# Kernel tuning notes

Measured on AMD Instinct MI355X. Metric: run time of the kernel, lower is better.

Reference implementation:

```python
import jax, jax.numpy as jnp
import numpy as np

N = 20000      # n_nodes
E = 320000     # n_edges (avg degree 16)
DIM = 64       # feature dim
HEADS = 4      # attention heads; per-head channel = DIM (PyG TransformerConv with concat=False)


def setup_inputs() -> dict:
    key = jax.random.key(0)
    ks = jax.random.split(key, 12)
    s = 0.05
    return {
        "f_mole": jax.random.normal(ks[0], (N, DIM), jnp.float32),
        "edge_weight": jax.random.uniform(ks[1], (E,), jnp.float32),
        "gcn_w": jax.random.normal(ks[2], (DIM, DIM), jnp.float32) * s,
        "gcn_b": jnp.zeros((DIM,), jnp.float32),
        "wq": jax.random.normal(ks[3], (DIM, HEADS * DIM), jnp.float32) * s,
        "bq": jnp.zeros((HEADS * DIM,), jnp.float32),
        "wk": jax.random.normal(ks[4], (DIM, HEADS * DIM), jnp.float32) * s,
        "bk": jnp.zeros((HEADS * DIM,), jnp.float32),
        "wv": jax.random.normal(ks[5], (DIM, HEADS * DIM), jnp.float32) * s,
        "bv": jnp.zeros((HEADS * DIM,), jnp.float32),
        "wskip": jax.random.normal(ks[6], (DIM, DIM), jnp.float32) * s,
        "bskip": jnp.zeros((DIM,), jnp.float32),
        "wbeta": jax.random.normal(ks[7], (3 * DIM, 1), jnp.float32) * s,
        "conv_w": jax.random.normal(ks[8], (DIM, DIM), jnp.float32) * s,  # Conv1d weight[o,0,k,0]
        "conv_b": jnp.zeros((DIM,), jnp.float32),
        "edges": jax.random.randint(ks[9], (2, E), 0, N, jnp.int32),
    }


def _forward(f_mole, edge_weight, gcn_w, gcn_b, wq, bq, wk, bk, wv, bv,
             wskip, bskip, wbeta, conv_w, conv_b, edges):
    n = f_mole.shape[0]
    dim = f_mole.shape[1]
    heads = wq.shape[1] // dim
    src, dst = edges[0], edges[1]  # PyG flow: source -> target

    # ---- GCNConv(dim, dim) with edge weights (add_self_loops=True, normalize=True) ----
    loops = jnp.arange(n, dtype=src.dtype)
    src_sl = jnp.concatenate([src, loops])
    dst_sl = jnp.concatenate([dst, loops])
    ew = jnp.concatenate([edge_weight, jnp.ones((n,), f_mole.dtype)])
    deg = jax.ops.segment_sum(ew, dst_sl, num_segments=n)
    dinv = jnp.where(deg > 0, jax.lax.rsqrt(deg), 0.0)
    norm = dinv[src_sl] * ew * dinv[dst_sl]              # (E+N,)
    xw = f_mole @ gcn_w                                   # (N, dim)
    agg = jax.ops.segment_sum(norm[:, None] * xw[src_sl], dst_sl, num_segments=n)
    f_gcn = jax.nn.relu(agg + gcn_b)                      # (N, dim)

    # ---- TransformerConv(dim, dim, heads, concat=False, beta=True) ----
    q = (f_gcn @ wq + bq).reshape(n, heads, dim)
    k = (f_gcn @ wk + bk).reshape(n, heads, dim)
    v = (f_gcn @ wv + bv).reshape(n, heads, dim)
    logits = jnp.einsum('ehc,ehc->eh', q[dst], k[src]) / jnp.sqrt(jnp.float32(dim))  # (E, H)
    m = jax.ops.segment_max(logits, dst, num_segments=n)  # (N, H)
    ex = jnp.exp(logits - m[dst])
    z = jax.ops.segment_sum(ex, dst, num_segments=n)      # (N, H)
    alpha = ex / z[dst]                                   # per-target softmax over edges
    out = jax.ops.segment_sum(alpha[:, :, None] * v[src], dst, num_segments=n)  # (N, H, dim)
    out = out.mean(axis=1)                                # concat=False -> head mean
    x_r = f_gcn @ wskip + bskip                           # root/skip branch
    beta = jax.nn.sigmoid(jnp.concatenate([out, x_r, out - x_r], axis=-1) @ wbeta)  # (N, 1)
    f_tf = jax.nn.relu(beta * x_r + (1.0 - beta) * out)   # (N, dim)

    # ---- Conv1d(1, dim, kernel_size=(dim,1)) on f_tf.T viewed as (1,1,dim,N) ----
    # out[o, n] = sum_k conv_w[o, k] * f_tf.T[k, n] + conv_b[o]  -> shape (1, dim, 1, N)
    conv = jnp.einsum('ok,nk->on', conv_w, f_tf) + conv_b[:, None]  # (dim, N)
    # torch .view(1, n_mole, -1) on (1, dim, 1, N): row-major reshape
    f_intra = conv.reshape(1, n, dim)
    return f_intra


def reference(f_mole, edge_weight, gcn_w, gcn_b, wq, bq, wk, bk, wv, bv,
              wskip, bskip, wbeta, conv_w, conv_b, edges):
    return _forward(f_mole, edge_weight, gcn_w, gcn_b, wq, bq, wk, bk, wv, bv,
                    wskip, bskip, wbeta, conv_w, conv_b, edges)
```

## Files before the change

kernel.cpp:

```cpp
#include <hip/hip_runtime.h>
#include <hip/hip_bf16.h>

#define DIM 64
#define HEADS 4
#define HD 256
#define CAP 64

typedef __attribute__((ext_vector_type(8))) short bf16x8;
typedef __attribute__((ext_vector_type(8))) unsigned short u16x8;
typedef __attribute__((ext_vector_type(4))) float f32x4;

template<int CTRL>
__device__ __forceinline__ float dpp_rot(float x) {
    return __int_as_float(__builtin_amdgcn_update_dpp(
        0, __float_as_int(x), CTRL, 0xF, 0xF, true));
}
__device__ __forceinline__ float reduce16(float x) {
    x += dpp_rot<0x121>(x);
    x += dpp_rot<0x122>(x);
    x += dpp_rot<0x124>(x);
    x += dpp_rot<0x128>(x);
    return x;
}
__device__ __forceinline__ unsigned short f2bf(float f) {
    unsigned u = __float_as_uint(f);
    unsigned r = (u + 0x7FFFu + ((u >> 16) & 1u)) >> 16;
    return (unsigned short)r;
}
__device__ __forceinline__ float bf2f(unsigned short u) {
    return __uint_as_float((unsigned)u << 16);
}

__global__ void scatter_all(const int* __restrict__ edges, const float* __restrict__ ew,
                            int* counts, int2* __restrict__ csr, int nE) {
    int e = blockIdx.x * blockDim.x + threadIdx.x;
    if (e < nE) {
        int dst = edges[nE + e];
        int src = edges[e];
        float w = ew[e];
        int p = atomicAdd(&counts[dst], 1);
        int2 rec;
        rec.x = src;
        rec.y = __float_as_int(w);
        csr[(dst << 6) + p] = rec;
    }
}

__global__ __launch_bounds__(256) void deg_dinv_k(const int* __restrict__ counts,
                                                  const int2* __restrict__ csr,
                                                  float* __restrict__ dinv, int n) {
    int i = blockIdx.x * 256 + threadIdx.x;
    if (i >= n) return;
    int c = counts[i];
    const int2* p = csr + ((size_t)i << 6);
    float s = 0.f;
    for (int j = 0; j < c; ++j) s += __int_as_float(p[j].y);
    dinv[i] = rsqrtf(s + 1.0f);
}

__device__ __forceinline__ void tile_load_A(float (*As)[68], const float* __restrict__ A,
                                            int row0, int n, int tid) {
    int c4 = (tid & 15) * 4;
    int sw = (tid & 7) << 2;
    #pragma unroll
    for (int it = 0; it < 4; ++it) {
        int r = (tid >> 4) + it * 16;
        float4 val = make_float4(0.f, 0.f, 0.f, 0.f);
        if (row0 + r < n)
            val = *reinterpret_cast<const float4*>(A + (size_t)(row0 + r) * DIM + c4);
        int rs = r ^ sw;
        As[c4 + 0][rs] = val.x;
        As[c4 + 1][rs] = val.y;
        As[c4 + 2][rs] = val.z;
        As[c4 + 3][rs] = val.w;
    }
}

__device__ __forceinline__ void tile_mm(const float (*As)[68], const float (*Bs)[68],
                                        float acc[4][4], int r0, int c0) {
    #pragma unroll 8
    for (int kk = 0; kk < 64; ++kk) {
        int sw = ((kk >> 2) & 7) << 2;
        float4 av = *reinterpret_cast<const float4*>(&As[kk][r0 ^ sw]);
        float4 bv = *reinterpret_cast<const float4*>(&Bs[kk][c0]);
        float a_[4] = {av.x, av.y, av.z, av.w};
        float b_[4] = {bv.x, bv.y, bv.z, bv.w};
        #pragma unroll
        for (int i = 0; i < 4; ++i)
            #pragma unroll
            for (int j = 0; j < 4; ++j)
                acc[i][j] += a_[i] * b_[j];
    }
}

__global__ __launch_bounds__(256) void gemm_xw(const float* __restrict__ A,
                                               const float* __restrict__ W,
                                               const float* __restrict__ dinv,
                                               unsigned short* __restrict__ out,
                                               int n) {
    __shared__ float As[64][68];
    __shared__ float Bs[64][68];
    int row0 = blockIdx.x * 64;
    int tid = threadIdx.x;
    tile_load_A(As, A, row0, n, tid);
    #pragma unroll
    for (int it = 0; it < 4; ++it) {
        int r  = (tid >> 4) + it * 16;
        int c4 = (tid & 15) * 4;
        *reinterpret_cast<float4*>(&Bs[r][c4]) =
            *reinterpret_cast<const float4*>(W + (size_t)r * DIM + c4);
    }
    __syncthreads();
    int r0 = (tid >> 4) * 4;
    int c0 = (tid & 15) * 4;
    float acc[4][4] = {};
    tile_mm(As, Bs, acc, r0, c0);
    #pragma unroll
    for (int i = 0; i < 4; ++i) {
        int r = row0 + r0 + i;
        if (r >= n) continue;
        float d = dinv[r];
        ushort4 u;
        u.x = f2bf(d * acc[i][0]); u.y = f2bf(d * acc[i][1]);
        u.z = f2bf(d * acc[i][2]); u.w = f2bf(d * acc[i][3]);
        *reinterpret_cast<ushort4*>(out + (size_t)r * DIM + c0) = u;
    }
}

__global__ __launch_bounds__(256) void gcn_agg(const unsigned short* __restrict__ xws,
                                               const int* __restrict__ counts,
                                               const int2* __restrict__ csr,
                                               const float* __restrict__ dinv,
                                               const float* __restrict__ gcn_b,
                                               unsigned short* __restrict__ f_gcnh, int n) {
    int wave = threadIdx.x >> 6;
    int lane = threadIdx.x & 63;
    int i = blockIdx.x * 4 + wave;
    if (i >= n) return;
    int eo = lane >> 4;
    int cg = lane & 15;

    float4 acc = make_float4(0.f, 0.f, 0.f, 0.f);
    int e0 = i << 6;
    int e1 = e0 + counts[i];
    int eb = e0;
    for (; eb + 16 <= e1; eb += 16) {
        int2 p[4];
        #pragma unroll
        for (int j = 0; j < 4; ++j) p[j] = csr[eb + 4 * j + eo];
        ushort4 x[4];
        #pragma unroll
        for (int j = 0; j < 4; ++j)
            x[j] = *reinterpret_cast<const ushort4*>(xws + (size_t)p[j].x * DIM + cg * 4);
        #pragma unroll
        for (int j = 0; j < 4; ++j) {
            float c = __int_as_float(p[j].y);
            acc.x += c * bf2f(x[j].x); acc.y += c * bf2f(x[j].y);
            acc.z += c * bf2f(x[j].z); acc.w += c * bf2f(x[j].w);
        }
    }
    for (int e = eb + eo; e < e1; e += 4) {
        int2 p = csr[e];
        float c = __int_as_float(p.y);
        ushort4 x4 = *reinterpret_cast<const ushort4*>(xws + (size_t)p.x * DIM + cg * 4);
        acc.x += c * bf2f(x4.x); acc.y += c * bf2f(x4.y);
        acc.z += c * bf2f(x4.z); acc.w += c * bf2f(x4.w);
    }
    acc.x += __shfl_xor(acc.x, 16, 64); acc.x += __shfl_xor(acc.x, 32, 64);
    acc.y += __shfl_xor(acc.y, 16, 64); acc.y += __shfl_xor(acc.y, 32, 64);
    acc.z += __shfl_xor(acc.z, 16, 64); acc.z += __shfl_xor(acc.z, 32, 64);
    acc.w += __shfl_xor(acc.w, 16, 64); acc.w += __shfl_xor(acc.w, 32, 64);

    float di = dinv[i];
    ushort4 xs = *reinterpret_cast<const ushort4*>(xws + (size_t)i * DIM + cg * 4);
    const float* b = gcn_b + cg * 4;
    if (eo == 0) {
        ushort4 u;
        u.x = f2bf(fmaxf(di * (acc.x + bf2f(xs.x)) + b[0], 0.f));
        u.y = f2bf(fmaxf(di * (acc.y + bf2f(xs.y)) + b[1], 0.f));
        u.z = f2bf(fmaxf(di * (acc.z + bf2f(xs.z)) + b[2], 0.f));
        u.w = f2bf(fmaxf(di * (acc.w + bf2f(xs.w)) + b[3], 0.f));
        *reinterpret_cast<ushort4*>(f_gcnh + (size_t)i * DIM + cg * 4) = u;
    }
}

__global__ __launch_bounds__(256) void qkv_mfma(const unsigned short* __restrict__ Ah,
        const float* __restrict__ wq, const float* __restrict__ bq,
        const float* __restrict__ wk, const float* __restrict__ bk,
        const float* __restrict__ wv, const float* __restrict__ bv,
        const float* __restrict__ wsk, const float* __restrict__ bsk,
        unsigned short* __restrict__ qo, unsigned short* __restrict__ kvb,
        float* __restrict__ xrb, int n) {
    int ty = blockIdx.y;
    const float* W; const float* bias; float scale = 1.0f;
    int ncw, mode;
    int col0 = (ty & 3) * 64;
    if (ty < 4)       { W = wq;  bias = bq;  ncw = HD;  mode = 0; scale = 0.125f; }
    else if (ty < 8)  { W = wk;  bias = bk;  ncw = HD;  mode = 1; }
    else if (ty < 12) { W = wv;  bias = bv;  ncw = HD;  mode = 2; }
    else              { W = wsk; bias = bsk; ncw = DIM; mode = 3; col0 = 0; }

    int row0 = blockIdx.x * 64;
    int wid  = threadIdx.x >> 6;
    int lane = threadIdx.x & 63;
    int hm = wid >> 1, hn = wid & 1;
    int lrow = lane & 15;
    int lk8  = (lane >> 4) * 8;

    bf16x8 afr[2][2];
    #pragma unroll
    for (int ks = 0; ks < 2; ++ks)
        #pragma unroll
        for (int fm = 0; fm < 2; ++fm) {
            int r = row0 + hm * 32 + fm * 16 + lrow;
            bf16x8 v8;
            if (r < n) {
                v8 = *reinterpret_cast<const bf16x8*>(Ah + (size_t)r * DIM + ks * 32 + lk8);
            } else {
                #pragma unroll
                for (int j = 0; j < 8; ++j) v8[j] = 0;
            }
            afr[ks][fm] = v8;
        }

    bf16x8 bfr[2][2];
    #pragma unroll
    for (int ks = 0; ks < 2; ++ks)
        #pragma unroll
        for (int fn = 0; fn < 2; ++fn) {
            int c = col0 + hn * 32 + fn * 16 + lrow;
            const float* wp = W + (size_t)(ks * 32 + lk8) * ncw + c;
            bf16x8 v8;
            #pragma unroll
            for (int j = 0; j < 8; ++j)
                v8[j] = (short)f2bf(wp[(size_t)j * ncw]);
            bfr[ks][fn] = v8;
        }

    f32x4 zz = {0.f, 0.f, 0.f, 0.f};
    f32x4 acc[2][2] = {{zz, zz}, {zz, zz}};
    #pragma unroll
    for (int ks = 0; ks < 2; ++ks)
        #pragma unroll
        for (int fm = 0; fm < 2; ++fm)
            #pragma unroll
            for (int fn = 0; fn < 2; ++fn)
                acc[fm][fn] = __builtin_amdgcn_mfma_f32_16x16x32_bf16(
                    afr[ks][fm], bfr[ks][fn], acc[fm][fn], 0, 0, 0);

    int drow = (lane >> 4) * 4;
    int dcol = lane & 15;
    #pragma unroll
    for (int fm = 0; fm < 2; ++fm)
        #pragma unroll
        for (int fn = 0; fn < 2; ++fn) {
            int col = col0 + hn * 32 + fn * 16 + dcol;
            float bcol = bias[col];
            #pragma unroll
            for (int r = 0; r < 4; ++r) {
                int row = row0 + hm * 32 + fm * 16 + drow + r;
                if (row >= n) continue;
                float val = (acc[fm][fn][r] + bcol) * scale;
                if (mode == 0) {
                    qo[(size_t)row * HD + col] = f2bf(val);
                } else if (mode == 3) {
                    xrb[(size_t)row * DIM + col] = val;
                } else {
                    int h = col >> 6, c6 = col & 63;
                    kvb[(size_t)row * 512 + h * 128 + (c6 >> 2) * 8 + (c6 & 3)
                        + (mode == 2 ? 4 : 0)] = f2bf(val);
                }
            }
        }
}

__global__ __launch_bounds__(256) void attn_fused(const unsigned short* __restrict__ q,
                                                  const unsigned short* __restrict__ kvb,
                                                  const float* __restrict__ x_r,
                                                  const int* __restrict__ counts,
                                                  const int2* __restrict__ csr,
                                                  const float* __restrict__ wbeta,
                                                  float* __restrict__ f_tf, int n) {
    int wave = threadIdx.x >> 6;
    int lane = threadIdx.x & 63;
    int i = blockIdx.x * 4 + wave;
    if (i >= n) return;
    int h  = lane >> 4;
    int cg = lane & 15;
    int kvoff = h * 128 + cg * 8;

    ushort4 qv = *reinterpret_cast<const ushort4*>(q + (size_t)i * HD + h * DIM + cg * 4);
    float4 q4;
    q4.x = bf2f(qv.x); q4.y = bf2f(qv.y); q4.z = bf2f(qv.z); q4.w = bf2f(qv.w);
    float z = 0.f;
    float4 a = make_float4(0.f, 0.f, 0.f, 0.f);

    int e0 = i << 6;
    int cnt = counts[i];
    int e1 = e0 + cnt;
    int e = e0;
    for (; e + 8 <= e1; e += 8) {
        int s[8];
        #pragma unroll
        for (int j = 0; j < 8; ++j) s[j] = csr[e + j].x;
        u16x8 kv[8];
        #pragma unroll
        for (int j = 0; j < 8; ++j)
            kv[j] = *reinterpret_cast<const u16x8*>(kvb + (size_t)s[j] * 512 + kvoff);
        float pl[8];
        #pragma unroll
        for (int j = 0; j < 8; ++j)
            pl[j] = q4.x * bf2f(kv[j][0]) + q4.y * bf2f(kv[j][1])
                  + q4.z * bf2f(kv[j][2]) + q4.w * bf2f(kv[j][3]);
        #pragma unroll
        for (int j = 0; j < 8; ++j) pl[j] = reduce16(pl[j]);
        #pragma unroll
        for (int j = 0; j < 8; ++j) {
            float ez = __expf(pl[j]);
            z += ez;
            a.x += ez * bf2f(kv[j][4]); a.y += ez * bf2f(kv[j][5]);
            a.z += ez * bf2f(kv[j][6]); a.w += ez * bf2f(kv[j][7]);
        }
    }
    for (; e + 4 <= e1; e += 4) {
        int s[4];
        #pragma unroll
        for (int j = 0; j < 4; ++j) s[j] = csr[e + j].x;
        u16x8 kv[4];
        #pragma unroll
        for (int j = 0; j < 4; ++j)
            kv[j] = *reinterpret_cast<const u16x8*>(kvb + (size_t)s[j] * 512 + kvoff);
        #pragma unroll
        for (int j = 0; j < 4; ++j) {
            float p = q4.x * bf2f(kv[j][0]) + q4.y * bf2f(kv[j][1])
                    + q4.z * bf2f(kv[j][2]) + q4.w * bf2f(kv[j][3]);
            p = reduce16(p);
            float ez = __expf(p);
            z += ez;
            a.x += ez * bf2f(kv[j][4]); a.y += ez * bf2f(kv[j][5]);
            a.z += ez * bf2f(kv[j][6]); a.w += ez * bf2f(kv[j][7]);
        }
    }
    for (; e < e1; ++e) {
        int s = csr[e].x;
        u16x8 kv = *reinterpret_cast<const u16x8*>(kvb + (size_t)s * 512 + kvoff);
        float p = q4.x * bf2f(kv[0]) + q4.y * bf2f(kv[1])
                + q4.z * bf2f(kv[2]) + q4.w * bf2f(kv[3]);
        p = reduce16(p);
        float ez = __expf(p);
        z += ez;
        a.x += ez * bf2f(kv[4]); a.y += ez * bf2f(kv[5]);
        a.z += ez * bf2f(kv[6]); a.w += ez * bf2f(kv[7]);
    }

    float inv = (cnt > 0) ? 1.0f / z : 0.f;
    float4 o;
    o.x = a.x * inv; o.y = a.y * inv; o.z = a.z * inv; o.w = a.w * inv;
    o.x += __shfl_xor(o.x, 16, 64); o.x += __shfl_xor(o.x, 32, 64);
    o.y += __shfl_xor(o.y, 16, 64); o.y += __shfl_xor(o.y, 32, 64);
    o.z += __shfl_xor(o.z, 16, 64); o.z += __shfl_xor(o.z, 32, 64);
    o.w += __shfl_xor(o.w, 16, 64); o.w += __shfl_xor(o.w, 32, 64);
    o.x *= 0.25f; o.y *= 0.25f; o.z *= 0.25f; o.w *= 0.25f;

    float4 xr4 = *reinterpret_cast<const float4*>(x_r + (size_t)i * DIM + cg * 4);
    const float* w1 = wbeta + cg * 4;
    const float* w2 = wbeta + 64 + cg * 4;
    const float* w3 = wbeta + 128 + cg * 4;
    float t = o.x * w1[0] + o.y * w1[1] + o.z * w1[2] + o.w * w1[3]
            + xr4.x * w2[0] + xr4.y * w2[1] + xr4.z * w2[2] + xr4.w * w2[3]
            + (o.x - xr4.x) * w3[0] + (o.y - xr4.y) * w3[1]
            + (o.z - xr4.z) * w3[2] + (o.w - xr4.w) * w3[3];
    t = reduce16(t);
    float beta = 1.0f / (1.0f + __expf(-t));
    float4 r;
    r.x = fmaxf(beta * xr4.x + (1.0f - beta) * o.x, 0.f);
    r.y = fmaxf(beta * xr4.y + (1.0f - beta) * o.y, 0.f);
    r.z = fmaxf(beta * xr4.z + (1.0f - beta) * o.z, 0.f);
    r.w = fmaxf(beta * xr4.w + (1.0f - beta) * o.w, 0.f);
    if (h == 0)
        *reinterpret_cast<float4*>(f_tf + (size_t)i * DIM + cg * 4) = r;
}

__global__ __launch_bounds__(256) void conv_out_k(const float* __restrict__ f_tf,
                                                  const float* __restrict__ conv_w,
                                                  const float* __restrict__ conv_b,
                                                  float* __restrict__ out, int n) {
    int nn = blockIdx.x * 256 + threadIdx.x;
    int ob = blockIdx.y * 16;
    if (nn >= n) return;
    float4 r4[16];
    #pragma unroll
    for (int j = 0; j < 16; ++j)
        r4[j] = *reinterpret_cast<const float4*>(f_tf + (size_t)nn * DIM + j * 4);
    #pragma unroll
    for (int oo = 0; oo < 16; ++oo) {
        int o = ob + oo;
        const float* wr = conv_w + (size_t)o * DIM;
        float acc = conv_b[o];
        #pragma unroll
        for (int j = 0; j < 16; ++j) {
            acc += r4[j].x * wr[j * 4 + 0] + r4[j].y * wr[j * 4 + 1] +
                   r4[j].z * wr[j * 4 + 2] + r4[j].w * wr[j * 4 + 3];
        }
        out[(size_t)o * n + nn] = acc;
    }
}

extern "C" void kernel_launch(void* const* d_in, const int* in_sizes, int n_in,
                              void* d_out, int out_size, void* d_ws, size_t ws_size,
                              hipStream_t stream) {
    const float* f_mole = (const float*)d_in[0];
    const float* edge_w = (const float*)d_in[1];
    const float* gcn_w  = (const float*)d_in[2];
    const float* gcn_b  = (const float*)d_in[3];
    const float* wq     = (const float*)d_in[4];
    const float* bq     = (const float*)d_in[5];
    const float* wk     = (const float*)d_in[6];
    const float* bk     = (const float*)d_in[7];
    const float* wv     = (const float*)d_in[8];
    const float* bv     = (const float*)d_in[9];
    const float* wskip  = (const float*)d_in[10];
    const float* bskip  = (const float*)d_in[11];
    const float* wbeta  = (const float*)d_in[12];
    const float* conv_w = (const float*)d_in[13];
    const float* conv_b = (const float*)d_in[14];
    const int*   edges  = (const int*)d_in[15];

    int N = in_sizes[0] / DIM;
    int E = in_sizes[1];

    float* ws = (float*)d_ws;
    size_t o = 0;
    int*   counts  = (int*)(ws + o); o += N;
    float* dinv    = ws + o;         o += N;
    int2*  csr     = (int2*)(ws + o); o += (size_t)2 * N * CAP;
    unsigned short* xws    = (unsigned short*)(ws + o); o += (size_t)N * DIM / 2;
    unsigned short* f_gcnh = (unsigned short*)(ws + o); o += (size_t)N * DIM / 2;
    unsigned short* qb     = (unsigned short*)(ws + o); o += (size_t)N * HD / 2;
    unsigned short* kvb    = (unsigned short*)(ws + o); o += (size_t)N * 512 / 2;
    float* xrb     = ws + o;         o += (size_t)N * DIM;
    float* ftf     = ws + o;         o += (size_t)N * DIM;

    int ebl = (E + 255) / 256;
    int nbl = (N + 255) / 256;
    int gbl = (N + 63) / 64;

    hipMemsetAsync(d_ws, 0, (size_t)N * sizeof(int), stream);
    scatter_all<<<ebl, 256, 0, stream>>>(edges, edge_w, counts, csr, E);
    deg_dinv_k<<<nbl, 256, 0, stream>>>(counts, csr, dinv, N);

    gemm_xw<<<gbl, 256, 0, stream>>>(f_mole, gcn_w, dinv, xws, N);
    gcn_agg<<<(N + 3) / 4, 256, 0, stream>>>(xws, counts, csr, dinv, gcn_b, f_gcnh, N);

    qkv_mfma<<<dim3(gbl, 13), 256, 0, stream>>>(f_gcnh, wq, bq, wk, bk, wv, bv,
                                                wskip, bskip, qb, kvb, xrb, N);

    attn_fused<<<(N + 3) / 4, 256, 0, stream>>>(qb, kvb, xrb, counts, csr, wbeta, ftf, N);
    conv_out_k<<<dim3(nbl, 4), 256, 0, stream>>>(ftf, conv_w, conv_b, (float*)d_out, N);
}
```

Baseline: 143.2 us.

## Pack CSR records into 32 bits and pre-transpose QKV weights to bf16

Each CSR entry is packed from an int2 into a single 32-bit word: a 16-bit source index plus an fp16 edge weight. This halves CSR storage and the traffic in the aggregation and attention kernels. The degree/dinv computation is folded into the xW GEMM kernel, removing a launch. A small kernel pre-converts the Q/K/V/skip weights to transposed bf16, so qkv_mfma does vector loads instead of strided fp32 loads with conversion. In exchange, node count is limited to 65536 and edge weights lose precision to fp16.

```diff
diff --git a/kernel.cpp b/kernel.cpp
--- a/kernel.cpp
+++ b/kernel.cpp
@@ -1,5 +1,6 @@
 #include <hip/hip_runtime.h>
 #include <hip/hip_bf16.h>
+#include <hip/hip_fp16.h>
 
 #define DIM 64
 #define HEADS 4
@@ -30,32 +31,41 @@
 __device__ __forceinline__ float bf2f(unsigned short u) {
     return __uint_as_float((unsigned)u << 16);
 }
+__device__ __forceinline__ float rec_w(unsigned rec) {
+    return __half2float(__ushort_as_half((unsigned short)(rec & 0xffffu)));
+}
 
 __global__ void scatter_all(const int* __restrict__ edges, const float* __restrict__ ew,
-                            int* counts, int2* __restrict__ csr, int nE) {
+                            int* counts, unsigned* __restrict__ csr, int nE) {
     int e = blockIdx.x * blockDim.x + threadIdx.x;
     if (e < nE) {
         int dst = edges[nE + e];
         int src = edges[e];
         float w = ew[e];
         int p = atomicAdd(&counts[dst], 1);
-        int2 rec;
-        rec.x = src;
-        rec.y = __float_as_int(w);
+        unsigned rec = ((unsigned)src << 16)
+                     | (unsigned)__half_as_ushort(__float2half(w));
         csr[(dst << 6) + p] = rec;
     }
 }
 
-__global__ __launch_bounds__(256) void deg_dinv_k(const int* __restrict__ counts,
-                                                  const int2* __restrict__ csr,
-                                                  float* __restrict__ dinv, int n) {
-    int i = blockIdx.x * 256 + threadIdx.x;
-    if (i >= n) return;
-    int c = counts[i];
-    const int2* p = csr + ((size_t)i << 6);
-    float s = 0.f;
-    for (int j = 0; j < c; ++j) s += __int_as_float(p[j].y);
-    dinv[i] = rsqrtf(s + 1.0f);
+__global__ __launch_bounds__(256) void wt_conv(const float* __restrict__ wq,
+                                               const float* __restrict__ wk,
+                                               const float* __restrict__ wv,
+                                               const float* __restrict__ wsk,
+                                               unsigned short* __restrict__ wt) {
+    int p = blockIdx.x;
+    const float* W; int ncw, col0;
+    if (p < 4)       { W = wq;  ncw = HD;  col0 = p * 64; }
+    else if (p < 8)  { W = wk;  ncw = HD;  col0 = (p - 4) * 64; }
+    else if (p < 12) { W = wv;  ncw = HD;  col0 = (p - 8) * 64; }
+    else             { W = wsk; ncw = DIM; col0 = 0; }
+    int c  = threadIdx.x >> 2;
+    int k0 = (threadIdx.x & 3) * 16;
+    unsigned short* out = wt + ((size_t)p * 64 + c) * 64 + k0;
+    #pragma unroll
+    for (int j = 0; j < 16; ++j)
+        out[j] = f2bf(W[(size_t)(k0 + j) * ncw + col0 + c]);
 }
 
 __device__ __forceinline__ void tile_load_A(float (*As)[68], const float* __restrict__ A,
@@ -95,13 +105,30 @@
 
 __global__ __launch_bounds__(256) void gemm_xw(const float* __restrict__ A,
                                                const float* __restrict__ W,
-                                               const float* __restrict__ dinv,
+                                               const int* __restrict__ counts,
+                                               const unsigned* __restrict__ csr,
+                                               float* __restrict__ dinv,
                                                unsigned short* __restrict__ out,
                                                int n) {
     __shared__ float As[64][68];
     __shared__ float Bs[64][68];
+    __shared__ float dloc[64];
     int row0 = blockIdx.x * 64;
     int tid = threadIdx.x;
+
+    if (tid < 64) {
+        int r = row0 + tid;
+        if (r < n) {
+            int c = counts[r];
+            const unsigned* p = csr + ((size_t)r << 6);
+            float s = 0.f;
+            for (int j = 0; j < c; ++j) s += rec_w(p[j]);
+            float d = rsqrtf(s + 1.0f);
+            dinv[r] = d;
+            dloc[tid] = d;
+        }
+    }
+
     tile_load_A(As, A, row0, n, tid);
     #pragma unroll
     for (int it = 0; it < 4; ++it) {
@@ -119,7 +146,7 @@
     for (int i = 0; i < 4; ++i) {
         int r = row0 + r0 + i;
         if (r >= n) continue;
-        float d = dinv[r];
+        float d = dloc[r0 + i];
         ushort4 u;
         u.x = f2bf(d * acc[i][0]); u.y = f2bf(d * acc[i][1]);
         u.z = f2bf(d * acc[i][2]); u.w = f2bf(d * acc[i][3]);
@@ -129,7 +156,7 @@
 
 __global__ __launch_bounds__(256) void gcn_agg(const unsigned short* __restrict__ xws,
                                                const int* __restrict__ counts,
-                                               const int2* __restrict__ csr,
+                                               const unsigned* __restrict__ csr,
                                                const float* __restrict__ dinv,
                                                const float* __restrict__ gcn_b,
                                                unsigned short* __restrict__ f_gcnh, int n) {
@@ -145,24 +172,24 @@
     int e1 = e0 + counts[i];
     int eb = e0;
     for (; eb + 16 <= e1; eb += 16) {
-        int2 p[4];
+        unsigned p[4];
         #pragma unroll
         for (int j = 0; j < 4; ++j) p[j] = csr[eb + 4 * j + eo];
         ushort4 x[4];
         #pragma unroll
         for (int j = 0; j < 4; ++j)
-            x[j] = *reinterpret_cast<const ushort4*>(xws + (size_t)p[j].x * DIM + cg * 4);
+            x[j] = *reinterpret_cast<const ushort4*>(xws + (size_t)(p[j] >> 16) * DIM + cg * 4);
         #pragma unroll
         for (int j = 0; j < 4; ++j) {
-            float c = __int_as_float(p[j].y);
+            float c = rec_w(p[j]);
             acc.x += c * bf2f(x[j].x); acc.y += c * bf2f(x[j].y);
             acc.z += c * bf2f(x[j].z); acc.w += c * bf2f(x[j].w);
         }
     }
     for (int e = eb + eo; e < e1; e += 4) {
-        int2 p = csr[e];
-        float c = __int_as_float(p.y);
-        ushort4 x4 = *reinterpret_cast<const ushort4*>(xws + (size_t)p.x * DIM + cg * 4);
+        unsigned p = csr[e];
+        float c = rec_w(p);
+        ushort4 x4 = *reinterpret_cast<const ushort4*>(xws + (size_t)(p >> 16) * DIM + cg * 4);
         acc.x += c * bf2f(x4.x); acc.y += c * bf2f(x4.y);
         acc.z += c * bf2f(x4.z); acc.w += c * bf2f(x4.w);
     }
@@ -185,20 +212,19 @@
 }
 
 __global__ __launch_bounds__(256) void qkv_mfma(const unsigned short* __restrict__ Ah,
-        const float* __restrict__ wq, const float* __restrict__ bq,
-        const float* __restrict__ wk, const float* __restrict__ bk,
-        const float* __restrict__ wv, const float* __restrict__ bv,
-        const float* __restrict__ wsk, const float* __restrict__ bsk,
+        const unsigned short* __restrict__ wt,
+        const float* __restrict__ bq, const float* __restrict__ bk,
+        const float* __restrict__ bv, const float* __restrict__ bsk,
         unsigned short* __restrict__ qo, unsigned short* __restrict__ kvb,
         float* __restrict__ xrb, int n) {
     int ty = blockIdx.y;
-    const float* W; const float* bias; float scale = 1.0f;
-    int ncw, mode;
+    const float* bias; float scale = 1.0f;
+    int mode;
     int col0 = (ty & 3) * 64;
-    if (ty < 4)       { W = wq;  bias = bq;  ncw = HD;  mode = 0; scale = 0.125f; }
-    else if (ty < 8)  { W = wk;  bias = bk;  ncw = HD;  mode = 1; }
-    else if (ty < 12) { W = wv;  bias = bv;  ncw = HD;  mode = 2; }
-    else              { W = wsk; bias = bsk; ncw = DIM; mode = 3; col0 = 0; }
+    if (ty < 4)       { bias = bq;  mode = 0; scale = 0.125f; }
+    else if (ty < 8)  { bias = bk;  mode = 1; }
+    else if (ty < 12) { bias = bv;  mode = 2; }
+    else              { bias = bsk; mode = 3; col0 = 0; }
 
     int row0 = blockIdx.x * 64;
     int wid  = threadIdx.x >> 6;
@@ -206,6 +232,7 @@
     int hm = wid >> 1, hn = wid & 1;
     int lrow = lane & 15;
     int lk8  = (lane >> 4) * 8;
+    const unsigned short* wtp = wt + (size_t)ty * 64 * 64;
 
     bf16x8 afr[2][2];
     #pragma unroll
@@ -228,13 +255,9 @@
     for (int ks = 0; ks < 2; ++ks)
         #pragma unroll
         for (int fn = 0; fn < 2; ++fn) {
-            int c = col0 + hn * 32 + fn * 16 + lrow;
-            const float* wp = W + (size_t)(ks * 32 + lk8) * ncw + c;
-            bf16x8 v8;
-            #pragma unroll
-            for (int j = 0; j < 8; ++j)
-                v8[j] = (short)f2bf(wp[(size_t)j * ncw]);
-            bfr[ks][fn] = v8;
+            int cl = hn * 32 + fn * 16 + lrow;
+            bfr[ks][fn] = *reinterpret_cast<const bf16x8*>(
+                wtp + (size_t)cl * 64 + ks * 32 + lk8);
         }
 
     f32x4 zz = {0.f, 0.f, 0.f, 0.f};
@@ -278,7 +301,7 @@
                                                   const unsigned short* __restrict__ kvb,
                                                   const float* __restrict__ x_r,
                                                   const int* __restrict__ counts,
-                                                  const int2* __restrict__ csr,
+                                                  const unsigned* __restrict__ csr,
                                                   const float* __restrict__ wbeta,
                                                   float* __restrict__ f_tf, int n) {
     int wave = threadIdx.x >> 6;
@@ -302,7 +325,7 @@
     for (; e + 8 <= e1; e += 8) {
         int s[8];
         #pragma unroll
-        for (int j = 0; j < 8; ++j) s[j] = csr[e + j].x;
+        for (int j = 0; j < 8; ++j) s[j] = (int)(csr[e + j] >> 16);
         u16x8 kv[8];
         #pragma unroll
         for (int j = 0; j < 8; ++j)
@@ -325,7 +348,7 @@
     for (; e + 4 <= e1; e += 4) {
         int s[4];
         #pragma unroll
-        for (int j = 0; j < 4; ++j) s[j] = csr[e + j].x;
+        for (int j = 0; j < 4; ++j) s[j] = (int)(csr[e + j] >> 16);
         u16x8 kv[4];
         #pragma unroll
         for (int j = 0; j < 4; ++j)
@@ -342,7 +365,7 @@
         }
     }
     for (; e < e1; ++e) {
-        int s = csr[e].x;
+        int s = (int)(csr[e] >> 16);
         u16x8 kv = *reinterpret_cast<const u16x8*>(kvb + (size_t)s * 512 + kvoff);
         float p = q4.x * bf2f(kv[0]) + q4.y * bf2f(kv[1])
                 + q4.z * bf2f(kv[2]) + q4.w * bf2f(kv[3]);
@@ -431,15 +454,16 @@
 
     float* ws = (float*)d_ws;
     size_t o = 0;
-    int*   counts  = (int*)(ws + o); o += N;
-    float* dinv    = ws + o;         o += N;
-    int2*  csr     = (int2*)(ws + o); o += (size_t)2 * N * CAP;
+    int*      counts = (int*)(ws + o);      o += N;
+    float*    dinv   = ws + o;              o += N;
+    unsigned* csr    = (unsigned*)(ws + o); o += (size_t)N * CAP;
+    unsigned short* wt     = (unsigned short*)(ws + o); o += (size_t)13 * 64 * 64 / 2;
     unsigned short* xws    = (unsigned short*)(ws + o); o += (size_t)N * DIM / 2;
     unsigned short* f_gcnh = (unsigned short*)(ws + o); o += (size_t)N * DIM / 2;
     unsigned short* qb     = (unsigned short*)(ws + o); o += (size_t)N * HD / 2;
     unsigned short* kvb    = (unsigned short*)(ws + o); o += (size_t)N * 512 / 2;
-    float* xrb     = ws + o;         o += (size_t)N * DIM;
-    float* ftf     = ws + o;         o += (size_t)N * DIM;
+    float* xrb = ws + o;                    o += (size_t)N * DIM;
+    float* ftf = ws + o;                    o += (size_t)N * DIM;
 
     int ebl = (E + 255) / 256;
     int nbl = (N + 255) / 256;
@@ -447,13 +471,13 @@
 
     hipMemsetAsync(d_ws, 0, (size_t)N * sizeof(int), stream);
     scatter_all<<<ebl, 256, 0, stream>>>(edges, edge_w, counts, csr, E);
-    deg_dinv_k<<<nbl, 256, 0, stream>>>(counts, csr, dinv, N);
-
-    gemm_xw<<<gbl, 256, 0, stream>>>(f_mole, gcn_w, dinv, xws, N);
+    wt_conv<<<13, 256, 0, stream>>>(wq, wk, wv, wskip, wt);
+
+    gemm_xw<<<gbl, 256, 0, stream>>>(f_mole, gcn_w, counts, csr, dinv, xws, N);
     gcn_agg<<<(N + 3) / 4, 256, 0, stream>>>(xws, counts, csr, dinv, gcn_b, f_gcnh, N);
 
-    qkv_mfma<<<dim3(gbl, 13), 256, 0, stream>>>(f_gcnh, wq, bq, wk, bk, wv, bv,
-                                                wskip, bskip, qb, kvb, xrb, N);
+    qkv_mfma<<<dim3(gbl, 13), 256, 0, stream>>>(f_gcnh, wt, bq, bk, bv, bskip,
+                                                qb, kvb, xrb, N);
 
     attn_fused<<<(N + 3) / 4, 256, 0, stream>>>(qb, kvb, xrb, counts, csr, wbeta, ftf, N);
     conv_out_k<<<dim3(nbl, 4), 256, 0, stream>>>(ftf, conv_w, conv_b, (float*)d_out, N);
```

After: 144.8 us. About the same (+1.1%).
